# Performance work log

Hardware: AMD Instinct MI355X
Metric: run time of the kernel (lower is better)

## Reference

```python
import jax, jax.numpy as jnp
import numpy as np

B = 8; NPB = 12500; N = B * NPB; DEG = 16; E = N * DEG
W_IMG, H_IMG = 240.0, 180.0
GX, GY = 15, 15
NC = GX * GY             # 225 clusters per sample
N2 = B * NC              # pooled node count (fixed)
CH = [1, 8, 8, 32, 32, 128]
NUM_OUT = 101
EPS = 1e-5


def _coarse_edges():
    # deterministic 8-neighborhood on the 15x15 pooled grid (torus), per sample
    gy, gx = np.meshgrid(np.arange(GY), np.arange(GX), indexing='ij')
    base = (gy * GX + gx).reshape(-1)
    srcs, dsts = [], []
    for dy in (-1, 0, 1):
        for dx in (-1, 0, 1):
            if dy == 0 and dx == 0:
                continue
            nb = (((gy + dy) % GY) * GX + (gx + dx) % GX).reshape(-1)
            srcs.append(nb); dsts.append(base)
    s = np.concatenate(srcs); d = np.concatenate(dsts)
    s = (s[None] + NC * np.arange(B)[:, None]).reshape(-1)
    d = (d[None] + NC * np.arange(B)[:, None]).reshape(-1)
    return np.stack([s, d]).astype(np.int32)


def setup_inputs():
    key = jax.random.key(0)
    ks = jax.random.split(key, 32)
    pos = jnp.concatenate([
        jax.random.uniform(ks[0], (N, 1)) * W_IMG,
        jax.random.uniform(ks[1], (N, 1)) * H_IMG,
        jax.random.uniform(ks[2], (N, 1))], axis=1)
    x = jax.random.normal(ks[3], (N, 1))
    batch = jnp.repeat(jnp.arange(B, dtype=jnp.int32), NPB)
    src = jax.random.randint(ks[4], (E,), 0, NPB, dtype=jnp.int32) + jnp.repeat(batch * NPB, DEG)
    dst = jnp.repeat(jnp.arange(N, dtype=jnp.int32), DEG)
    inp = {'x': x, 'pos': pos, 'batch': batch,
           'edge_index': jnp.stack([src, dst]),
           'edge_index2': jnp.asarray(_coarse_edges())}
    ki = 5
    for l in range(5):
        cin, cout = CH[l], CH[l + 1]
        for nm, fan in (('w_lin', cin), ('w_src', cin), ('w_dst', cin), ('w_pos', 3)):
            inp[f'{nm}{l+1}'] = jax.random.normal(ks[ki], (fan, cout)) / np.sqrt(fan)
            ki += 1
        inp[f'b_pos{l+1}'] = jnp.zeros((cout,))
        inp[f'g{l+1}'] = jnp.ones((cout,))
        inp[f'be{l+1}'] = jnp.zeros((cout,))
    inp['w_fc'] = jax.random.normal(ks[ki], (CH[5] * 16, NUM_OUT)) * 0.02
    return inp


def pt_conv(x, pos, src, dst, n_nodes, w_lin, w_src, w_dst, w_pos, b_pos):
    # PyG PointTransformerConv with add_self_loops=True, sum aggregation
    loops = jnp.arange(n_nodes, dtype=src.dtype)
    src = jnp.concatenate([src, loops]); dst = jnp.concatenate([dst, loops])
    h = x @ w_lin                           # value transform [N, cout]
    a_src = x @ w_src; a_dst = x @ w_dst
    delta = (pos[dst] - pos[src]) @ w_pos + b_pos      # pos_nn(pos_i - pos_j)
    alpha = a_dst[dst] - a_src[src] + delta            # [E, cout]
    amax = jax.ops.segment_max(alpha, dst, num_segments=n_nodes)
    amax = jnp.where(jnp.isneginf(amax), 0.0, amax)
    ex = jnp.exp(alpha - amax[dst])
    denom = jax.ops.segment_sum(ex, dst, num_segments=n_nodes)
    attn = ex / (denom[dst] + 1e-16)
    msg = attn * (h[src] + delta)
    return jax.ops.segment_sum(msg, dst, num_segments=n_nodes)


def bn(x, g, b):
    mu = x.mean(0)
    var = x.var(0)
    return g * (x - mu) * jax.lax.rsqrt(var + EPS) + b


def pool3(x, pos, batch):
    # voxel-grid max pool (16,12), fixed N2 clusters; pos -> cluster mean
    cx = jnp.clip(jnp.floor(pos[:, 0] / 16.0).astype(jnp.int32), 0, GX - 1)
    cy = jnp.clip(jnp.floor(pos[:, 1] / 12.0).astype(jnp.int32), 0, GY - 1)
    cl = batch * NC + cy * GX + cx
    x2 = jax.ops.segment_max(x, cl, num_segments=N2)
    x2 = jnp.where(jnp.isneginf(x2), 0.0, x2)
    cnt = jax.ops.segment_sum(jnp.ones((pos.shape[0], 1), pos.dtype), cl, num_segments=N2)
    pos2 = jax.ops.segment_sum(pos, cl, num_segments=N2) / jnp.maximum(cnt, 1.0)
    return x2, pos2


def pool5(x2, pos2):
    # MaxPoolingX: 4x4 grid (cell size 60x45), 16 clusters per sample
    batch2 = jnp.arange(N2, dtype=jnp.int32) // NC
    cx = jnp.clip(jnp.floor(pos2[:, 0] / (W_IMG / 4)).astype(jnp.int32), 0, 3)
    cy = jnp.clip(jnp.floor(pos2[:, 1] / (H_IMG / 4)).astype(jnp.int32), 0, 3)
    cl = batch2 * 16 + cy * 4 + cx
    out = jax.ops.segment_max(x2, cl, num_segments=B * 16)
    out = jnp.where(jnp.isneginf(out), 0.0, out)
    return out.reshape(B, 16 * CH[5])


def _forward(x, pos, batch, edge_index, edge_index2, convs, bns, w_fc):
    src, dst = edge_index[0], edge_index[1]
    h = bn(jax.nn.elu(pt_conv(x, pos, src, dst, N, *convs[0])), *bns[0])
    sc = h
    h = bn(jax.nn.elu(pt_conv(h, pos, src, dst, N, *convs[1])), *bns[1]) + sc
    h = bn(jax.nn.elu(pt_conv(h, pos, src, dst, N, *convs[2])), *bns[2])
    h2, pos2 = pool3(h, pos, batch)
    s2, d2 = edge_index2[0], edge_index2[1]
    sc = h2
    h2 = bn(jax.nn.elu(pt_conv(h2, pos2, s2, d2, N2, *convs[3])), *bns[3]) + sc
    h2 = bn(jax.nn.elu(pt_conv(h2, pos2, s2, d2, N2, *convs[4])), *bns[4])
    return pool5(h2, pos2) @ w_fc


def reference(x, pos, batch, edge_index, edge_index2,
              w_lin1, w_src1, w_dst1, w_pos1, b_pos1, g1, be1,
              w_lin2, w_src2, w_dst2, w_pos2, b_pos2, g2, be2,
              w_lin3, w_src3, w_dst3, w_pos3, b_pos3, g3, be3,
              w_lin4, w_src4, w_dst4, w_pos4, b_pos4, g4, be4,
              w_lin5, w_src5, w_dst5, w_pos5, b_pos5, g5, be5,
              w_fc):
    convs = [(w_lin1, w_src1, w_dst1, w_pos1, b_pos1),
             (w_lin2, w_src2, w_dst2, w_pos2, b_pos2),
             (w_lin3, w_src3, w_dst3, w_pos3, b_pos3),
             (w_lin4, w_src4, w_dst4, w_pos4, b_pos4),
             (w_lin5, w_src5, w_dst5, w_pos5, b_pos5)]
    bns = [(g1, be1), (g2, be2), (g3, be3), (g4, be4), (g5, be5)]
    return _forward(x, pos, batch, edge_index, edge_index2, convs, bns, w_fc)
```

## Files before the change

### kernel.cpp

```cpp
#include <hip/hip_runtime.h>

#define ENC_NEGINF 0x007FFFFFu
#define NN_FINE 100000
#define NN_COARSE 1800
#define INV_N  (1.0f / 100000.0f)
#define INV_N2 (1.0f / 1800.0f)

__device__ __forceinline__ unsigned enc_f(float f) {
    unsigned u = __float_as_uint(f);
    return (u & 0x80000000u) ? ~u : (u | 0x80000000u);
}
__device__ __forceinline__ float dec_f(unsigned k) {
    return (k & 0x80000000u) ? __uint_as_float(k & 0x7fffffffu) : __uint_as_float(~k);
}

__device__ __forceinline__ int xcd_swz(int bid, int nwg) {
    int q = nwg >> 3, r = nwg & 7;
    int xcd = bid & 7, idx = bid >> 3;
    return (xcd < r ? xcd * (q + 1) : r * (q + 1) + (xcd - r) * q) + idx;
}

__device__ __forceinline__ float2 bn_ss(const float* __restrict__ st,
                                        const float* __restrict__ g,
                                        const float* __restrict__ be,
                                        int r, float invn) {
    float mu  = st[r] * invn;
    float var = fmaxf(st[128 + r] * invn - mu * mu, 0.f);
    float s = g[r] * rsqrtf(var + 1e-5f);
    return make_float2(s, be[r] - mu * s);
}

template<int CIN, int COUT, int MODE>
__global__ void pass_a(const float* __restrict__ in,
                       const float* __restrict__ st, const float* __restrict__ g,
                       const float* __restrict__ be, float invn,
                       const float* __restrict__ skipf,
                       const float* __restrict__ wl, const float* __restrict__ wsrc,
                       const float* __restrict__ wpos, const float* __restrict__ bpos,
                       const float* __restrict__ pos,
                       float4* __restrict__ SHP, float2* __restrict__ CAP,
                       float* __restrict__ zout, int total,
                       float* __restrict__ zstats, float* __restrict__ zo) {
    constexpr int P = COUT / 2;
    int idx = blockIdx.x * blockDim.x + threadIdx.x;
    if (zstats) {
        if (idx < 1280) zstats[idx] = 0.f;
        if (idx < 808)  zo[idx] = 0.f;
    }
    if (idx >= total) return;
    int i = idx / P, p = idx % P;
    float f[CIN];
#pragma unroll
    for (int r = 0; r < CIN; ++r) {
        float v = in[i * CIN + r];
        if constexpr (MODE >= 1) {
            float2 ss = bn_ss(st, g, be, r, invn);
            v = v * ss.x + ss.y;
        }
        if constexpr (MODE == 2) v += skipf[i * CIN + r];
        f[r] = v;
    }
    int c0 = 2 * p;
    float h0 = 0.f, a0 = 0.f, h1 = 0.f, a1 = 0.f;
#pragma unroll
    for (int r = 0; r < CIN; ++r) {
        float2 wlr = *reinterpret_cast<const float2*>(&wl[r * COUT + c0]);
        float2 wsr = *reinterpret_cast<const float2*>(&wsrc[r * COUT + c0]);
        h0 += f[r] * wlr.x; h1 += f[r] * wlr.y;
        a0 += f[r] * wsr.x; a1 += f[r] * wsr.y;
    }
    float px = pos[i * 3], py = pos[i * 3 + 1], pz = pos[i * 3 + 2];
    float2 w0 = *reinterpret_cast<const float2*>(&wpos[c0]);
    float2 w1 = *reinterpret_cast<const float2*>(&wpos[COUT + c0]);
    float2 w2 = *reinterpret_cast<const float2*>(&wpos[2 * COUT + c0]);
    float pd0 = px * w0.x + py * w1.x + pz * w2.x;
    float pd1 = px * w0.y + py * w1.y + pz * w2.y;
    float2 bp = *reinterpret_cast<const float2*>(&bpos[c0]);
    SHP[(size_t)i * P + p] = make_float4(a0 + pd0, a1 + pd1, h0 - pd0, h1 - pd1);
    CAP[(size_t)i * P + p] = make_float2(pd0 + bp.x, pd1 + bp.y);
    if constexpr (MODE == 1) {
        float2 s0 = bn_ss(st, g, be, c0, invn);
        float2 s1 = bn_ss(st, g, be, c0 + 1, invn);
        float2 zv = make_float2(in[i * CIN + c0] * s0.x + s0.y,
                                in[i * CIN + c0 + 1] * s1.x + s1.y);
        *reinterpret_cast<float2*>(&zout[i * CIN + c0]) = zv;
    }
}

template<int C, bool COARSE>
__global__ __launch_bounds__(256, 4)
void edge_pass(const float4* __restrict__ SHP, const float2* __restrict__ CAP,
               const int* __restrict__ esrc, float2* __restrict__ y2,
               float* __restrict__ PS, int NN) {
    constexpr int P = C / 2;
    constexpr int NPB = 256 / P;
    constexpr int DEG_ = COARSE ? 8 : 16;
    __shared__ int se[NPB * DEG_];
    __shared__ float ls[C], lq[C];
    int bid = COARSE ? (int)blockIdx.x : xcd_swz(blockIdx.x, gridDim.x);
    int tid = threadIdx.x;
    int node0 = bid * NPB;
    if constexpr (!COARSE) {
        for (int t = tid; t < NPB * DEG_; t += 256)
            se[t] = esrc[node0 * 16 + t];
    } else {
        for (int t = tid; t < NPB * DEG_; t += 256) {
            int n = t / DEG_, e = t % DEG_;
            int i2 = node0 + n;
            if (i2 < NN) {
                int b = i2 / 225, j = i2 % 225;
                se[t] = esrc[b * 1800 + e * 225 + j];
            }
        }
    }
    if (tid < C) { ls[tid] = 0.f; lq[tid] = 0.f; }
    __syncthreads();
    int n = tid / P, p = tid % P;
    int i = node0 + n;
    float y0 = 0.f, y1 = 0.f;
    if (i < NN) {
        float4 q[DEG_ + 1];
#pragma unroll
        for (int e = 0; e < DEG_; ++e)
            q[e] = SHP[(size_t)se[n * DEG_ + e] * P + p];
        q[DEG_] = SHP[(size_t)i * P + p];

        float smin0 = q[0].x, smin1 = q[0].y;
#pragma unroll
        for (int e = 1; e <= DEG_; ++e) {
            smin0 = fminf(smin0, q[e].x);
            smin1 = fminf(smin1, q[e].y);
        }
        float den0 = 0.f, acc0 = 0.f, den1 = 0.f, acc1 = 0.f;
#pragma unroll
        for (int e = 0; e <= DEG_; ++e) {
            float ex0 = __expf(smin0 - q[e].x);
            float ex1 = __expf(smin1 - q[e].y);
            den0 += ex0; acc0 += ex0 * q[e].z;
            den1 += ex1; acc1 += ex1 * q[e].w;
        }
        float2 Ci = CAP[(size_t)i * P + p];
        float o0 = (acc0 + Ci.x * den0) / (den0 + 1e-16f);
        float o1 = (acc1 + Ci.y * den1) / (den1 + 1e-16f);
        y0 = o0 > 0.f ? o0 : (__expf(o0) - 1.f);
        y1 = o1 > 0.f ? o1 : (__expf(o1) - 1.f);
        y2[(size_t)i * P + p] = make_float2(y0, y1);
    }
    float sa0 = y0, sq0 = y0 * y0, sa1 = y1, sq1 = y1 * y1;
    if constexpr (P < 64) {
#pragma unroll
        for (int m = P; m < 64; m <<= 1) {
            sa0 += __shfl_xor(sa0, m); sa1 += __shfl_xor(sa1, m);
            sq0 += __shfl_xor(sq0, m); sq1 += __shfl_xor(sq1, m);
        }
    }
    if ((tid & 63) < P) {
        int c0 = 2 * p;
        atomicAdd(&ls[c0], sa0); atomicAdd(&ls[c0 + 1], sa1);
        atomicAdd(&lq[c0], sq0); atomicAdd(&lq[c0 + 1], sq1);
    }
    __syncthreads();
    if (tid < C) {
        if constexpr (COARSE) {
            atomicAdd(&PS[tid], ls[tid]);
            atomicAdd(&PS[128 + tid], lq[tid]);
        } else {
            PS[(size_t)blockIdx.x * 2 * C + tid]     = ls[tid];
            PS[(size_t)blockIdx.x * 2 * C + C + tid] = lq[tid];
        }
    }
}

template<int C>
__global__ __launch_bounds__(256)
void stats_r(const float* __restrict__ PS, int nb, float* __restrict__ STATS) {
    constexpr int TC = 2 * C;
    constexpr int NS = 256 / TC;
    __shared__ float acc[256];
    int tid = threadIdx.x;
    int c = tid % TC, sl = tid / TC;
    float s = 0.f;
    for (int b = blockIdx.x * NS + sl; b < nb; b += gridDim.x * NS)
        s += PS[(size_t)b * TC + c];
    acc[tid] = s;
    __syncthreads();
    if (tid < TC) {
        float t = 0.f;
#pragma unroll
        for (int s2 = 0; s2 < NS; ++s2) t += acc[s2 * TC + tid];
        float* dst = (tid < C) ? &STATS[tid] : &STATS[128 + (tid - C)];
        atomicAdd(dst, t);
    }
}

__global__ __launch_bounds__(256)
void pool3a(const float* __restrict__ y3, const float* __restrict__ pos,
            const float* __restrict__ PS, float* __restrict__ ST3,
            unsigned* __restrict__ PK, float* __restrict__ PC,
            float* __restrict__ PP) {
    __shared__ unsigned lkey[7200];
    __shared__ float lcnt[225];
    __shared__ float lpac[675];
    __shared__ float sacc[256];
    int tid = threadIdx.x;
    int bid = blockIdx.x;
    if (bid < 8) {
        int r0 = bid * 782, r1 = min(6250, r0 + 782);
        int c = tid & 63, qr = tid >> 6;
        float s = 0.f;
        for (int r = r0 + qr; r < r1; r += 4)
            s += PS[(size_t)r * 64 + c];
        sacc[tid] = s;
        __syncthreads();
        if (tid < 64) {
            float t = sacc[tid] + sacc[64 + tid] + sacc[128 + tid] + sacc[192 + tid];
            atomicAdd((tid < 32) ? &ST3[tid] : &ST3[128 + (tid - 32)], t);
        }
        __syncthreads();
    }
    for (int t = tid; t < 7200; t += 256) lkey[t] = ENC_NEGINF;
    if (tid < 225) lcnt[tid] = 0.f;
    for (int t = tid; t < 675; t += 256) lpac[t] = 0.f;
    __syncthreads();
    int s = bid >> 5, sb = bid & 31;
    int beg = s * 12500 + sb * 391;
    int end = min(s * 12500 + 12500, beg + 391);
    int c = tid & 31, nl = tid >> 5;
    for (int i = beg + nl; i < end; i += 8) {
        float z = y3[(size_t)i * 32 + c];
        float px = pos[i * 3], py = pos[i * 3 + 1];
        int cx = min(max((int)floorf(px / 16.f), 0), 14);
        int cy = min(max((int)floorf(py / 12.f), 0), 14);
        int cl = cy * 15 + cx;
        atomicMax(&lkey[cl * 32 + c], enc_f(z));
        if (c == 0) {
            atomicAdd(&lcnt[cl], 1.f);
            atomicAdd(&lpac[cl * 3 + 0], px);
            atomicAdd(&lpac[cl * 3 + 1], py);
            atomicAdd(&lpac[cl * 3 + 2], pos[i * 3 + 2]);
        }
    }
    __syncthreads();
    for (int t = tid; t < 7200; t += 256) PK[(size_t)bid * 7200 + t] = lkey[t];
    if (tid < 225) PC[bid * 225 + tid] = lcnt[tid];
    for (int t = tid; t < 675; t += 256) PP[bid * 675 + t] = lpac[t];
}

__global__ __launch_bounds__(256)
void p3b_a4(const unsigned* __restrict__ PK, const float* __restrict__ PC,
            const float* __restrict__ PP, const float* __restrict__ ST3,
            const float* __restrict__ g3, const float* __restrict__ be3,
            float* __restrict__ X2, float* __restrict__ POS2,
            const float* __restrict__ wl, const float* __restrict__ wsrc,
            const float* __restrict__ wpos, const float* __restrict__ bpos,
            float4* __restrict__ SHPc, float2* __restrict__ CAPc) {
    __shared__ float x2l[16 * 33];
    __shared__ float pos2l[48];
    int tid = threadIdx.x, blk = blockIdx.x;
    int nb0 = blk * 16;
    for (int t = tid; t < 512; t += 256) {
        int nl = t >> 5, c = t & 31;
        int n = nb0 + nl;
        if (n < NN_COARSE) {
            int s = n / 225, loc = n % 225;
            unsigned m = ENC_NEGINF;
#pragma unroll 8
            for (int sb = 0; sb < 32; ++sb)
                m = max(m, PK[(size_t)(s * 32 + sb) * 7200 + loc * 32 + c]);
            float2 ss = bn_ss(ST3, g3, be3, c, INV_N);
            float v = (m == ENC_NEGINF) ? 0.f : (dec_f(m) * ss.x + ss.y);
            x2l[nl * 33 + c] = v;
            X2[n * 32 + c] = v;
        }
    }
    if (tid < 48) {
        int nl = tid / 3, r = tid % 3;
        int n = nb0 + nl;
        if (n < NN_COARSE) {
            int s = n / 225, loc = n % 225;
            float sp = 0.f, sc = 0.f;
#pragma unroll 8
            for (int sb = 0; sb < 32; ++sb) {
                sp += PP[(s * 32 + sb) * 675 + loc * 3 + r];
                sc += PC[(s * 32 + sb) * 225 + loc];
            }
            float v = sp / fmaxf(sc, 1.f);
            pos2l[tid] = v;
            POS2[n * 3 + r] = v;
        }
    }
    __syncthreads();
    {
        int nl = tid >> 4, p = tid & 15;
        int n = nb0 + nl;
        if (n < NN_COARSE) {
            int c0 = 2 * p;
            float h0 = 0.f, a0 = 0.f, h1 = 0.f, a1 = 0.f;
#pragma unroll
            for (int r = 0; r < 32; ++r) {
                float fv = x2l[nl * 33 + r];
                float2 wlr = *reinterpret_cast<const float2*>(&wl[r * 32 + c0]);
                float2 wsr = *reinterpret_cast<const float2*>(&wsrc[r * 32 + c0]);
                h0 += fv * wlr.x; h1 += fv * wlr.y;
                a0 += fv * wsr.x; a1 += fv * wsr.y;
            }
            float px = pos2l[nl * 3], py = pos2l[nl * 3 + 1], pz = pos2l[nl * 3 + 2];
            float2 w0 = *reinterpret_cast<const float2*>(&wpos[c0]);
            float2 w1 = *reinterpret_cast<const float2*>(&wpos[32 + c0]);
            float2 w2 = *reinterpret_cast<const float2*>(&wpos[64 + c0]);
            float pd0 = px * w0.x + py * w1.x + pz * w2.x;
            float pd1 = px * w0.y + py * w1.y + pz * w2.y;
            float2 bp = *reinterpret_cast<const float2*>(&bpos[c0]);
            SHPc[(size_t)n * 16 + p] = make_float4(a0 + pd0, a1 + pd1, h0 - pd0, h1 - pd1);
            CAPc[(size_t)n * 16 + p] = make_float2(pd0 + bp.x, pd1 + bp.y);
        }
    }
}

__global__ __launch_bounds__(1024)
void pool5_k(const float* __restrict__ y5, const float* __restrict__ st,
             const float* __restrict__ g, const float* __restrict__ be,
             const float* __restrict__ POS2, float* __restrict__ POOLED) {
    __shared__ unsigned lkey[2048];
    int tid = threadIdx.x, s = blockIdx.x;
    for (int t = tid; t < 2048; t += 1024) lkey[t] = ENC_NEGINF;
    __syncthreads();
    int c = tid & 127, nl = tid >> 7;
    float2 ss = bn_ss(st, g, be, c, INV_N2);
    for (int j = nl; j < 225; j += 8) {
        int i = s * 225 + j;
        float z = y5[(size_t)i * 128 + c] * ss.x + ss.y;
        float px = POS2[i * 3], py = POS2[i * 3 + 1];
        int cx = min(max((int)floorf(px / 60.f), 0), 3);
        int cy = min(max((int)floorf(py / 45.f), 0), 3);
        atomicMax(&lkey[(cy * 4 + cx) * 128 + c], enc_f(z));
    }
    __syncthreads();
    for (int t = tid; t < 2048; t += 1024) {
        unsigned k = lkey[t];
        POOLED[s * 2048 + t] = (k == ENC_NEGINF) ? 0.f : dec_f(k);
    }
}

__global__ __launch_bounds__(256)
void fc_k(const float* __restrict__ POOLED, const float* __restrict__ wfc,
          float* __restrict__ out) {
    __shared__ float row[128];
    __shared__ float acc[256];
    int s = blockIdx.x, kc = blockIdx.y;
    int k0 = kc * 128;
    int tid = threadIdx.x;
    if (tid < 128) row[tid] = POOLED[s * 2048 + k0 + tid];
    __syncthreads();
    int o = tid & 127, half = tid >> 7;
    float a = 0.f;
    if (o < 101) {
        int kk0 = half * 64;
        for (int kk = kk0; kk < kk0 + 64; ++kk)
            a += row[kk] * wfc[(size_t)(k0 + kk) * 101 + o];
    }
    acc[tid] = a;
    __syncthreads();
    if (tid < 128 && o < 101)
        atomicAdd(&out[s * 101 + o], acc[tid] + acc[tid + 128]);
}

extern "C" void kernel_launch(void* const* d_in, const int* in_sizes, int n_in,
                              void* d_out, int out_size, void* d_ws, size_t ws_size,
                              hipStream_t stream) {
    const float* x     = (const float*)d_in[0];
    const float* pos   = (const float*)d_in[1];
    const int*   e1    = (const int*)d_in[3];
    const int*   e2    = (const int*)d_in[4];
    const float* w_fc  = (const float*)d_in[40];
    auto F = [&](int idx) { return (const float*)d_in[idx]; };

    float* W = (float*)d_ws;
    size_t o = 0;
    float4* SHPf = (float4*)W;        o += 6400000;
    float2* CAPf = (float2*)(W + o);  o += 3200000;
    float*  Y1   = W + o;             o += 800000;
    float*  Y2   = W + o;             o += 800000;
    float*  Z1   = W + o;             o += 800000;
    float*  Y3   = W + o;             o += 3200000;
    float*  STATS = W + o;            o += 5 * 256;
    float*  X2   = W + o;             o += 57600;
    float*  POS2 = W + o;             o += 5400;
    float4* SHPc = (float4*)(W + o);  o += 460800;
    float2* CAPc = (float2*)(W + o);  o += 230400;
    float*  Y4   = W + o;             o += 57600;
    float*  Y5   = W + o;             o += 230400;
    float*  POOLED = W + o;           o += 16384;
    float*  PSTAT  = W + o;           o += 400000;
    unsigned* PK = (unsigned*)W;
    float*    PC = W + 2000000;
    float*    PP = W + 2100000;

    hipLaunchKernelGGL((pass_a<1, 8, 0>), dim3(1563), dim3(256), 0, stream,
                       x, nullptr, nullptr, nullptr, 0.f, nullptr,
                       F(5), F(6), F(8), F(9), pos, SHPf, CAPf, nullptr, 400000,
                       STATS, (float*)d_out);
    hipLaunchKernelGGL((edge_pass<8, false>), dim3(1563), dim3(256), 0, stream,
                       SHPf, CAPf, e1, (float2*)Y1, PSTAT, NN_FINE);
    hipLaunchKernelGGL((stats_r<8>), dim3(32), dim3(256), 0, stream,
                       PSTAT, 1563, STATS + 0);

    hipLaunchKernelGGL((pass_a<8, 8, 1>), dim3(1563), dim3(256), 0, stream,
                       Y1, STATS + 0, F(10), F(11), INV_N, nullptr,
                       F(12), F(13), F(15), F(16), pos, SHPf, CAPf, Z1, 400000,
                       nullptr, nullptr);
    hipLaunchKernelGGL((edge_pass<8, false>), dim3(1563), dim3(256), 0, stream,
                       SHPf, CAPf, e1, (float2*)Y2, PSTAT, NN_FINE);
    hipLaunchKernelGGL((stats_r<8>), dim3(32), dim3(256), 0, stream,
                       PSTAT, 1563, STATS + 256);

    hipLaunchKernelGGL((pass_a<8, 32, 2>), dim3(6250), dim3(256), 0, stream,
                       Y2, STATS + 256, F(17), F(18), INV_N, Z1,
                       F(19), F(20), F(22), F(23), pos, SHPf, CAPf, nullptr, 1600000,
                       nullptr, nullptr);
    hipLaunchKernelGGL((edge_pass<32, false>), dim3(6250), dim3(256), 0, stream,
                       SHPf, CAPf, e1, (float2*)Y3, PSTAT, NN_FINE);

    hipLaunchKernelGGL(pool3a, dim3(256), dim3(256), 0, stream,
                       Y3, pos, PSTAT, STATS + 512, PK, PC, PP);

    hipLaunchKernelGGL(p3b_a4, dim3(113), dim3(256), 0, stream,
                       PK, PC, PP, STATS + 512, F(24), F(25), X2, POS2,
                       F(26), F(27), F(29), F(30), SHPc, CAPc);

    hipLaunchKernelGGL((edge_pass<32, true>), dim3(113), dim3(256), 0, stream,
                       SHPc, CAPc, e2, (float2*)Y4, STATS + 768, NN_COARSE);

    hipLaunchKernelGGL((pass_a<32, 128, 2>), dim3(450), dim3(256), 0, stream,
                       Y4, STATS + 768, F(31), F(32), INV_N2, X2,
                       F(33), F(34), F(36), F(37), POS2, SHPc, CAPc, nullptr, 115200,
                       nullptr, nullptr);
    hipLaunchKernelGGL((edge_pass<128, true>), dim3(450), dim3(256), 0, stream,
                       SHPc, CAPc, e2, (float2*)Y5, STATS + 1024, NN_COARSE);

    hipLaunchKernelGGL(pool5_k, dim3(8), dim3(1024), 0, stream,
                       Y5, STATS + 1024, F(38), F(39), POS2, POOLED);
    hipLaunchKernelGGL(fc_k, dim3(8, 16), dim3(256), 0, stream,
                       POOLED, w_fc, (float*)d_out);
}
```

Baseline: 246.7 us.

## Replace coarse-stage stat atomics with per-block partials and double pool3 grid

Coarse edge passes now write per-block BN partial sums instead of atomically accumulating into global stats. A dedicated a5_k kernel reduces layer-4 partials and fuses BN, residual and linear projections. stats_r kernels are added for layers 3 and 5. pool3a drops its embedded stats reduction and runs 512 blocks of 196 nodes instead of 256 of 391, so more blocks do scatter-max work while p3b reads twice as many partial buffers. This trades global atomic contention for extra small kernel launches and larger partial-buffer reads.

Result: faster. 228.1 us (-7.5%).

```diff
diff --git a/kernel.cpp b/kernel.cpp
--- a/kernel.cpp
+++ b/kernel.cpp
@@ -161,13 +161,8 @@
     }
     __syncthreads();
     if (tid < C) {
-        if constexpr (COARSE) {
-            atomicAdd(&PS[tid], ls[tid]);
-            atomicAdd(&PS[128 + tid], lq[tid]);
-        } else {
-            PS[(size_t)blockIdx.x * 2 * C + tid]     = ls[tid];
-            PS[(size_t)blockIdx.x * 2 * C + C + tid] = lq[tid];
-        }
+        PS[(size_t)blockIdx.x * 2 * C + tid]     = ls[tid];
+        PS[(size_t)blockIdx.x * 2 * C + C + tid] = lq[tid];
     }
 }
 
@@ -195,36 +190,20 @@
 
 __global__ __launch_bounds__(256)
 void pool3a(const float* __restrict__ y3, const float* __restrict__ pos,
-            const float* __restrict__ PS, float* __restrict__ ST3,
             unsigned* __restrict__ PK, float* __restrict__ PC,
             float* __restrict__ PP) {
     __shared__ unsigned lkey[7200];
     __shared__ float lcnt[225];
     __shared__ float lpac[675];
-    __shared__ float sacc[256];
     int tid = threadIdx.x;
-    int bid = blockIdx.x;
-    if (bid < 8) {
-        int r0 = bid * 782, r1 = min(6250, r0 + 782);
-        int c = tid & 63, qr = tid >> 6;
-        float s = 0.f;
-        for (int r = r0 + qr; r < r1; r += 4)
-            s += PS[(size_t)r * 64 + c];
-        sacc[tid] = s;
-        __syncthreads();
-        if (tid < 64) {
-            float t = sacc[tid] + sacc[64 + tid] + sacc[128 + tid] + sacc[192 + tid];
-            atomicAdd((tid < 32) ? &ST3[tid] : &ST3[128 + (tid - 32)], t);
-        }
-        __syncthreads();
-    }
     for (int t = tid; t < 7200; t += 256) lkey[t] = ENC_NEGINF;
     if (tid < 225) lcnt[tid] = 0.f;
     for (int t = tid; t < 675; t += 256) lpac[t] = 0.f;
     __syncthreads();
-    int s = bid >> 5, sb = bid & 31;
-    int beg = s * 12500 + sb * 391;
-    int end = min(s * 12500 + 12500, beg + 391);
+    int bid = blockIdx.x;
+    int s = bid >> 6, sb = bid & 63;
+    int beg = s * 12500 + sb * 196;
+    int end = min(s * 12500 + 12500, beg + 196);
     int c = tid & 31, nl = tid >> 5;
     for (int i = beg + nl; i < end; i += 8) {
         float z = y3[(size_t)i * 32 + c];
@@ -265,8 +244,8 @@
             int s = n / 225, loc = n % 225;
             unsigned m = ENC_NEGINF;
 #pragma unroll 8
-            for (int sb = 0; sb < 32; ++sb)
-                m = max(m, PK[(size_t)(s * 32 + sb) * 7200 + loc * 32 + c]);
+            for (int sb = 0; sb < 64; ++sb)
+                m = max(m, PK[(size_t)(s * 64 + sb) * 7200 + loc * 32 + c]);
             float2 ss = bn_ss(ST3, g3, be3, c, INV_N);
             float v = (m == ENC_NEGINF) ? 0.f : (dec_f(m) * ss.x + ss.y);
             x2l[nl * 33 + c] = v;
@@ -280,9 +259,9 @@
             int s = n / 225, loc = n % 225;
             float sp = 0.f, sc = 0.f;
 #pragma unroll 8
-            for (int sb = 0; sb < 32; ++sb) {
-                sp += PP[(s * 32 + sb) * 675 + loc * 3 + r];
-                sc += PC[(s * 32 + sb) * 225 + loc];
+            for (int sb = 0; sb < 64; ++sb) {
+                sp += PP[(s * 64 + sb) * 675 + loc * 3 + r];
+                sc += PC[(s * 64 + sb) * 225 + loc];
             }
             float v = sp / fmaxf(sc, 1.f);
             pos2l[tid] = v;
@@ -315,6 +294,59 @@
             CAPc[(size_t)n * 16 + p] = make_float2(pd0 + bp.x, pd1 + bp.y);
         }
     }
+}
+
+__global__ __launch_bounds__(256)
+void a5_k(const float* __restrict__ PS, const float* __restrict__ g4,
+          const float* __restrict__ be4, const float* __restrict__ Y4,
+          const float* __restrict__ X2,
+          const float* __restrict__ wl, const float* __restrict__ wsrc,
+          const float* __restrict__ wpos, const float* __restrict__ bpos,
+          const float* __restrict__ POS2,
+          float4* __restrict__ SHPc, float2* __restrict__ CAPc) {
+    __shared__ float red[64];
+    __shared__ float2 ssl[32];
+    int tid = threadIdx.x;
+    if (tid < 64) {
+        float s = 0.f;
+#pragma unroll 4
+        for (int r = 0; r < 113; ++r) s += PS[r * 64 + tid];
+        red[tid] = s;
+    }
+    __syncthreads();
+    if (tid < 32) {
+        float mu = red[tid] * INV_N2;
+        float var = fmaxf(red[32 + tid] * INV_N2 - mu * mu, 0.f);
+        float sc = g4[tid] * rsqrtf(var + 1e-5f);
+        ssl[tid] = make_float2(sc, be4[tid] - mu * sc);
+    }
+    __syncthreads();
+    int u = blockIdx.x * 256 + tid;
+    int i = u >> 6, p = u & 63;
+    float f[32];
+#pragma unroll
+    for (int r = 0; r < 32; ++r) {
+        float2 ss = ssl[r];
+        f[r] = Y4[i * 32 + r] * ss.x + ss.y + X2[i * 32 + r];
+    }
+    int c0 = 2 * p;
+    float h0 = 0.f, a0 = 0.f, h1 = 0.f, a1 = 0.f;
+#pragma unroll
+    for (int r = 0; r < 32; ++r) {
+        float2 wlr = *reinterpret_cast<const float2*>(&wl[r * 128 + c0]);
+        float2 wsr = *reinterpret_cast<const float2*>(&wsrc[r * 128 + c0]);
+        h0 += f[r] * wlr.x; h1 += f[r] * wlr.y;
+        a0 += f[r] * wsr.x; a1 += f[r] * wsr.y;
+    }
+    float px = POS2[i * 3], py = POS2[i * 3 + 1], pz = POS2[i * 3 + 2];
+    float2 w0 = *reinterpret_cast<const float2*>(&wpos[c0]);
+    float2 w1 = *reinterpret_cast<const float2*>(&wpos[128 + c0]);
+    float2 w2 = *reinterpret_cast<const float2*>(&wpos[256 + c0]);
+    float pd0 = px * w0.x + py * w1.x + pz * w2.x;
+    float pd1 = px * w0.y + py * w1.y + pz * w2.y;
+    float2 bp = *reinterpret_cast<const float2*>(&bpos[c0]);
+    SHPc[(size_t)i * 64 + p] = make_float4(a0 + pd0, a1 + pd1, h0 - pd0, h1 - pd1);
+    CAPc[(size_t)i * 64 + p] = make_float2(pd0 + bp.x, pd1 + bp.y);
 }
 
 __global__ __launch_bounds__(1024)
@@ -393,8 +425,8 @@
     float*  POOLED = W + o;           o += 16384;
     float*  PSTAT  = W + o;           o += 400000;
     unsigned* PK = (unsigned*)W;
-    float*    PC = W + 2000000;
-    float*    PP = W + 2100000;
+    float*    PC = W + 5600000;
+    float*    PP = W + 5800000;
 
     hipLaunchKernelGGL((pass_a<1, 8, 0>), dim3(1563), dim3(256), 0, stream,
                        x, nullptr, nullptr, nullptr, 0.f, nullptr,
@@ -420,23 +452,27 @@
                        nullptr, nullptr);
     hipLaunchKernelGGL((edge_pass<32, false>), dim3(6250), dim3(256), 0, stream,
                        SHPf, CAPf, e1, (float2*)Y3, PSTAT, NN_FINE);
-
-    hipLaunchKernelGGL(pool3a, dim3(256), dim3(256), 0, stream,
-                       Y3, pos, PSTAT, STATS + 512, PK, PC, PP);
+    hipLaunchKernelGGL((stats_r<32>), dim3(32), dim3(256), 0, stream,
+                       PSTAT, 6250, STATS + 512);
+
+    hipLaunchKernelGGL(pool3a, dim3(512), dim3(256), 0, stream,
+                       Y3, pos, PK, PC, PP);
 
     hipLaunchKernelGGL(p3b_a4, dim3(113), dim3(256), 0, stream,
                        PK, PC, PP, STATS + 512, F(24), F(25), X2, POS2,
                        F(26), F(27), F(29), F(30), SHPc, CAPc);
 
     hipLaunchKernelGGL((edge_pass<32, true>), dim3(113), dim3(256), 0, stream,
-                       SHPc, CAPc, e2, (float2*)Y4, STATS + 768, NN_COARSE);
-
-    hipLaunchKernelGGL((pass_a<32, 128, 2>), dim3(450), dim3(256), 0, stream,
-                       Y4, STATS + 768, F(31), F(32), INV_N2, X2,
-                       F(33), F(34), F(36), F(37), POS2, SHPc, CAPc, nullptr, 115200,
-                       nullptr, nullptr);
+                       SHPc, CAPc, e2, (float2*)Y4, PSTAT, NN_COARSE);
+
+    hipLaunchKernelGGL(a5_k, dim3(450), dim3(256), 0, stream,
+                       PSTAT, F(31), F(32), Y4, X2,
+                       F(33), F(34), F(36), F(37), POS2, SHPc, CAPc);
+
     hipLaunchKernelGGL((edge_pass<128, true>), dim3(450), dim3(256), 0, stream,
-                       SHPc, CAPc, e2, (float2*)Y5, STATS + 1024, NN_COARSE);
+                       SHPc, CAPc, e2, (float2*)Y5, PSTAT, NN_COARSE);
+    hipLaunchKernelGGL((stats_r<128>), dim3(16), dim3(256), 0, stream,
+                       PSTAT, 450, STATS + 1024);
 
     hipLaunchKernelGGL(pool5_k, dim3(8), dim3(1024), 0, stream,
                        Y5, STATS + 1024, F(38), F(39), POS2, POOLED);
```
